# Kernel optimization log

Hardware: AMD Instinct MI355X
Metric: run time of the kernel (lower is better)

The kernel has to match this reference:

```python
import jax, jax.numpy as jnp
import numpy as np

B, D, U = 4096, 256, 512


def setup_inputs() -> dict:
    key = jax.random.key(0)
    k = jax.random.split(key, 7)
    return {
        "x": jax.random.normal(k[0], (B, D), jnp.float32),
        "t": jax.random.uniform(k[1], (B, 1), jnp.float32),           # elapsed-time input
        "h0": jax.random.normal(k[2], (B, U), jnp.float32),
        "c0": jax.random.normal(k[3], (B, U), jnp.float32),
        "kernel": jax.random.normal(k[4], (D, 5 * U), jnp.float32) / np.sqrt(D).astype(np.float32),
        "recurrent_kernel": jax.random.normal(k[5], (U, 3 * U), jnp.float32) / np.sqrt(U).astype(np.float32),
        "kernel_time": jax.random.normal(k[6], (1, 3 * U), jnp.float32) * 0.1,
    }


def reference(x, t, h0, c0, kernel, recurrent_kernel, kernel_time):
    sig = jax.nn.sigmoid
    # Fused input projection: one GEMM instead of 5 (same math, kernel cols are
    # ordered [i, c, o, t1, t2] exactly as the original slices self.kernel).
    x_i, x_c, x_o, x_t1, x_t2 = jnp.split(x @ kernel, 5, axis=1)          # each (B, U)
    # Fused recurrent projection: cols ordered [i, c, o].
    r_i, r_c, r_o = jnp.split(h0 @ recurrent_kernel, 3, axis=1)           # each (B, U)
    # Time projections: cols ordered [t1, t2, o].
    kt1, kt2, kto = jnp.split(t @ kernel_time, 3, axis=1)                 # each (B, U)

    i = sig(x_i + r_i)
    t_1 = sig(x_t1 + sig(kt1))
    # tf.where(t_1 > -1e-5, -1e-5, t_1): sigmoid output is always > -1e-5,
    # so this clamps to the constant -1e-5; keep the where for faithfulness.
    NEG_EPS = jnp.float32(-1e-5)
    t_1_constraint = jnp.where(t_1 > NEG_EPS, jnp.full_like(t_1, NEG_EPS), t_1)
    t_2 = sig(x_t2 + sig(kt2))
    c_tilde = jnp.tanh(x_c + r_c)
    c_m_ = (1.0 - i * t_1) * c0 + i * c_tilde * t_1_constraint
    c_m = (1.0 - i) * c0 + i * c_tilde * t_2
    o = sig(x_o + r_o + kto)
    h = jnp.tanh(c_m_) * o
    # original returns (h, [h, c_m]); h appears twice, so return (h, c_m)
    return (h, c_m)
```

## Files before the change

### kernel.cpp

```cpp
#include <hip/hip_runtime.h>


typedef __attribute__((ext_vector_type(8))) short short8_t;
typedef __attribute__((ext_vector_type(4))) float f32x4_t;
typedef unsigned int u32;

#define B_N 4096
#define D_K 256
#define U_N 512

__device__ __forceinline__ unsigned short f2bf(float f) {
    unsigned int x = __float_as_uint(f);
    unsigned int r = x + 0x7fffu + ((x >> 16) & 1u);
    return (unsigned short)(r >> 16);
}

__device__ __forceinline__ float sigf(float z) {
    return 1.0f / (1.0f + __expf(-z));
}

__device__ __forceinline__ float tanhfast(float z) {
    return 1.0f - 2.0f / (1.0f + __expf(2.0f * z));
}

__device__ __forceinline__ void gl16(const unsigned short* g, unsigned short* l) {
    __builtin_amdgcn_global_load_lds(
        (const __attribute__((address_space(1))) u32*)g,
        (__attribute__((address_space(3))) u32*)l, 16, 0, 0);
}

#define SWZ(r, kc) ((((r) * 8) + ((kc) ^ ((r) & 7))) * 8)

#define WAIT_VM(N)                                            \
    asm volatile("s_waitcnt vmcnt(" #N ")" ::: "memory");     \
    __builtin_amdgcn_sched_barrier(0)

__global__ __launch_bounds__(256) void prep(
    const float* __restrict__ x, const float* __restrict__ h0,
    const float* __restrict__ kern, const float* __restrict__ rk,
    unsigned short* __restrict__ xs, unsigned short* __restrict__ hs,
    unsigned short* __restrict__ ksw, unsigned short* __restrict__ rsw)
{
    const int c = blockIdx.x * 256 + threadIdx.x;
    if (c < 131072) {
        const int t = c >> 10, q = c & 1023;
        const int row = q >> 3, kc = q & 7;
        const int rb = t >> 2, kb = t & 3;
        const float* s = x + (size_t)(rb * 128 + row) * D_K + kb * 64 + kc * 8;
        short8_t o;
#pragma unroll
        for (int j = 0; j < 8; ++j) o[j] = (short)f2bf(s[j]);
        *reinterpret_cast<short8_t*>(xs + (size_t)t * 8192 + SWZ(row, kc)) = o;
    } else if (c < 393216) {
        const int c2 = c - 131072;
        const int t = c2 >> 10, q = c2 & 1023;
        const int row = q >> 3, kc = q & 7;
        const int rb = t >> 3, kb = t & 7;
        const float* s = h0 + (size_t)(rb * 128 + row) * U_N + kb * 64 + kc * 8;
        short8_t o;
#pragma unroll
        for (int j = 0; j < 8; ++j) o[j] = (short)f2bf(s[j]);
        *reinterpret_cast<short8_t*>(hs + (size_t)t * 8192 + SWZ(row, kc)) = o;
    } else if (c < 475136) {
        const int c2 = c - 393216;
        const int t = c2 / 1280, q = c2 - t * 1280;
        const int kc = q / 160, r = q - kc * 160;
        const int nb = t >> 2, kb = t & 3;
        const int col = (r >> 5) * U_N + nb * 32 + (r & 31);
        short8_t o;
#pragma unroll
        for (int j = 0; j < 8; ++j)
            o[j] = (short)f2bf(kern[(size_t)(kb * 64 + kc * 8 + j) * 2560 + col]);
        *reinterpret_cast<short8_t*>(ksw + (size_t)t * 10240 + SWZ(r, kc)) = o;
    } else {
        const int c2 = c - 475136;
        const int t = c2 / 768, q = c2 - t * 768;
        const int kc = q / 96, r = q - kc * 96;
        const int nb = t >> 3, kb = t & 7;
        const int col = (r >> 5) * U_N + nb * 32 + (r & 31);
        short8_t o;
#pragma unroll
        for (int j = 0; j < 8; ++j)
            o[j] = (short)f2bf(rk[(size_t)(kb * 64 + kc * 8 + j) * 1536 + col]);
        *reinterpret_cast<short8_t*>(rsw + (size_t)t * 6144 + SWZ(r, kc)) = o;
    }
}

__global__ __launch_bounds__(512, 2) void tlstm_main(
    const unsigned short* __restrict__ xs,
    const unsigned short* __restrict__ hs,
    const unsigned short* __restrict__ ksw,
    const unsigned short* __restrict__ rsw,
    const float* __restrict__ tvec,
    const float* __restrict__ c0,
    const float* __restrict__ ktime,
    float* __restrict__ out)
{
    __shared__ __align__(16) unsigned short lds[2][28672];

    const int tid = threadIdx.x;
    const int wave = tid >> 6;
    const int lane = tid & 63;
    const int lr = lane & 15;
    const int lq = lane >> 4;
    const int wm = wave >> 2;
    const int wn = wave & 3;
    const int nb = blockIdx.x;
    const int rb = blockIdx.y;

    const int u = nb * 64 + wn * 16 + lr;

    f32x4_t acc[8][4];
#pragma unroll
    for (int m = 0; m < 8; ++m)
#pragma unroll
        for (int p = 0; p < 4; ++p)
            acc[m][p] = (f32x4_t){0.f, 0.f, 0.f, 0.f};

    float c0r[16];

    auto stage = [&](int s, int buf) {
        unsigned short* ab = &lds[buf][0];
        unsigned short* bb = &lds[buf][8192];
        if (s < 4) {
            const unsigned short* at = xs + (size_t)(rb * 4 + s) * 8192;
            gl16(at + (size_t)tid * 8,         ab + (size_t)(wave * 64) * 8);
            gl16(at + (size_t)(512 + tid) * 8, ab + (size_t)(512 + wave * 64) * 8);
            const unsigned short* b0 = ksw + (size_t)(nb * 8 + s) * 10240;
            const unsigned short* b1 = ksw + (size_t)(nb * 8 + 4 + s) * 10240;
#pragma unroll
            for (int j = 0; j < 5; ++j) {
                const int c = j * 512 + tid;
                const unsigned short* src = (c < 1280) ? (b0 + (size_t)c * 8)
                                                       : (b1 + (size_t)(c - 1280) * 8);
                gl16(src, bb + (size_t)(j * 512 + wave * 64) * 8);
            }
        } else {
            const unsigned short* at = hs + (size_t)(rb * 8 + (s - 4)) * 8192;
            gl16(at + (size_t)tid * 8,         ab + (size_t)(wave * 64) * 8);
            gl16(at + (size_t)(512 + tid) * 8, ab + (size_t)(512 + wave * 64) * 8);
            const unsigned short* b0 = rsw + (size_t)(nb * 16 + (s - 4)) * 6144;
            const unsigned short* b1 = rsw + (size_t)(nb * 16 + 8 + (s - 4)) * 6144;
#pragma unroll
            for (int j = 0; j < 3; ++j) {
                const int c = j * 512 + tid;
                const unsigned short* src = (c < 768) ? (b0 + (size_t)c * 8)
                                                      : (b1 + (size_t)(c - 768) * 8);
                gl16(src, bb + (size_t)(j * 512 + wave * 64) * 8);
            }
        }
    };

    auto compute1 = [&](int buf) {
        const unsigned short* ab = &lds[buf][0];
        const unsigned short* bb = &lds[buf][8192];
#pragma unroll
        for (int ks = 0; ks < 2; ++ks) {
            const int kc = ks * 4 + lq;
            short8_t a[4];
#pragma unroll
            for (int p = 0; p < 4; ++p)
                a[p] = *reinterpret_cast<const short8_t*>(ab + SWZ(wm * 64 + p * 16 + lr, kc));
#pragma unroll
            for (int m = 0; m < 5; ++m) {
                const int r = (wn >> 1) * 160 + m * 32 + (wn & 1) * 16 + lr;
                short8_t b = *reinterpret_cast<const short8_t*>(bb + SWZ(r, kc));
#pragma unroll
                for (int p = 0; p < 4; ++p)
                    acc[m][p] = __builtin_amdgcn_mfma_f32_16x16x32_bf16(a[p], b, acc[m][p], 0, 0, 0);
            }
        }
    };

    auto compute2 = [&](int buf) {
        const unsigned short* ab = &lds[buf][0];
        const unsigned short* bb = &lds[buf][8192];
#pragma unroll
        for (int ks = 0; ks < 2; ++ks) {
            const int kc = ks * 4 + lq;
            short8_t a[4];
#pragma unroll
            for (int p = 0; p < 4; ++p)
                a[p] = *reinterpret_cast<const short8_t*>(ab + SWZ(wm * 64 + p * 16 + lr, kc));
#pragma unroll
            for (int m = 0; m < 3; ++m) {
                const int r = (wn >> 1) * 96 + m * 32 + (wn & 1) * 16 + lr;
                short8_t b = *reinterpret_cast<const short8_t*>(bb + SWZ(r, kc));
#pragma unroll
                for (int p = 0; p < 4; ++p)
                    acc[5 + m][p] = __builtin_amdgcn_mfma_f32_16x16x32_bf16(a[p], b, acc[5 + m][p], 0, 0, 0);
            }
        }
    };

#define K_BODY(S, NV, CF)                                  \
    {                                                      \
        WAIT_VM(NV);                                       \
        __builtin_amdgcn_s_barrier();                      \
        __builtin_amdgcn_sched_barrier(0);                 \
        CF((S) & 1);                                       \
        __builtin_amdgcn_sched_barrier(0);                 \
        __builtin_amdgcn_s_barrier();                      \
        __builtin_amdgcn_sched_barrier(0);                 \
    }

    stage(0, 0);
    stage(1, 1);  K_BODY(0, 7,  compute1);
    stage(2, 0);  K_BODY(1, 7,  compute1);
    stage(3, 1);  K_BODY(2, 7,  compute1);
    stage(4, 0);  K_BODY(3, 5,  compute1);
    stage(5, 1);  K_BODY(4, 5,  compute2);
    stage(6, 0);  K_BODY(5, 5,  compute2);
    stage(7, 1);  K_BODY(6, 5,  compute2);
    stage(8, 0);  K_BODY(7, 5,  compute2);
    stage(9, 1);
    asm volatile("" ::: "memory");
#pragma unroll
    for (int p = 0; p < 4; ++p)
#pragma unroll
        for (int i2 = 0; i2 < 4; ++i2) {
            const int b = rb * 128 + wm * 64 + p * 16 + lq * 4 + i2;
            c0r[p * 4 + i2] = c0[(size_t)b * U_N + u];
        }
    K_BODY(8, 21, compute2);
    stage(10, 0); K_BODY(9, 21, compute2);
    stage(11, 1); K_BODY(10, 5, compute2);
    K_BODY(11, 0, compute2);

    const float NEG_EPS = -1e-5f;
    const float kt1 = ktime[u];
    const float kt2 = ktime[U_N + u];
    const float kto = ktime[2 * U_N + u];
#pragma unroll
    for (int p = 0; p < 4; ++p)
#pragma unroll
        for (int i2 = 0; i2 < 4; ++i2) {
            const int b = rb * 128 + wm * 64 + p * 16 + lq * 4 + i2;
            const float tb = tvec[b];
            const float c0v = c0r[p * 4 + i2];
            const float x_i  = acc[0][p][i2];
            const float x_c  = acc[1][p][i2];
            const float x_o  = acc[2][p][i2];
            const float x_t1 = acc[3][p][i2];
            const float x_t2 = acc[4][p][i2];
            const float r_i  = acc[5][p][i2];
            const float r_c  = acc[6][p][i2];
            const float r_o  = acc[7][p][i2];

            const float ig  = sigf(x_i + r_i);
            const float t1v = sigf(x_t1 + sigf(tb * kt1));
            const float t1c = (t1v > NEG_EPS) ? NEG_EPS : t1v;
            const float t2v = sigf(x_t2 + sigf(tb * kt2));
            const float ct  = tanhfast(x_c + r_c);
            const float cm_ = (1.f - ig * t1v) * c0v + ig * ct * t1c;
            const float cm  = (1.f - ig) * c0v + ig * ct * t2v;
            const float og  = sigf(x_o + r_o + tb * kto);

            out[(size_t)b * U_N + u] = tanhfast(cm_) * og;
            out[(size_t)B_N * U_N + (size_t)b * U_N + u] = cm;
        }
}

extern "C" void kernel_launch(void* const* d_in, const int* in_sizes, int n_in,
                              void* d_out, int out_size, void* d_ws, size_t ws_size,
                              hipStream_t stream) {
    const float* x     = (const float*)d_in[0];
    const float* t     = (const float*)d_in[1];
    const float* h0    = (const float*)d_in[2];
    const float* c0    = (const float*)d_in[3];
    const float* kern  = (const float*)d_in[4];
    const float* rk    = (const float*)d_in[5];
    const float* ktime = (const float*)d_in[6];
    float* out = (float*)d_out;

    unsigned short* xs  = (unsigned short*)d_ws;
    unsigned short* hs  = (unsigned short*)((char*)d_ws + 2097152);
    unsigned short* ksw = (unsigned short*)((char*)d_ws + 6291456);
    unsigned short* rsw = (unsigned short*)((char*)d_ws + 7602176);

    prep<<<2240, 256, 0, stream>>>(x, h0, kern, rk, xs, hs, ksw, rsw);
    tlstm_main<<<dim3(8, 32), 512, 0, stream>>>(
        xs, hs, ksw, rsw, t, c0, ktime, out);
}
```

Baseline: 35.80 us.

## Split MFMA k-steps into ping-pong phases with barriers and setprio

Each staged tile's compute is split into two k-phases. Each phase loads all of its LDS fragments up front, then a workgroup barrier and an lgkmcnt wait precede an MFMA burst raised with s_setprio, a ping-pong schedule meant to interleave LDS reads and MFMAs across waves. The c0 prefetch into registers mid-pipeline is dropped in favour of loading c0 directly in the epilogue, which simplifies the vmcnt waits but exposes c0 load latency at the end. The constant-folded t1 clamp removes a compare, and the extra barriers add synchronisation cost.

```diff
diff --git a/kernel.cpp b/kernel.cpp
--- a/kernel.cpp
+++ b/kernel.cpp
@@ -33,6 +33,14 @@
 
 #define WAIT_VM(N)                                            \
     asm volatile("s_waitcnt vmcnt(" #N ")" ::: "memory");     \
+    __builtin_amdgcn_sched_barrier(0)
+
+#define LGKM0                                                 \
+    asm volatile("s_waitcnt lgkmcnt(0)" ::: "memory");        \
+    __builtin_amdgcn_sched_barrier(0)
+
+#define SBAR                                                  \
+    __builtin_amdgcn_s_barrier();                             \
     __builtin_amdgcn_sched_barrier(0)
 
 __global__ __launch_bounds__(256) void prep(
@@ -117,8 +125,6 @@
         for (int p = 0; p < 4; ++p)
             acc[m][p] = (f32x4_t){0.f, 0.f, 0.f, 0.f};
 
-    float c0r[16];
-
     auto stage = [&](int s, int buf) {
         unsigned short* ab = &lds[buf][0];
         unsigned short* bb = &lds[buf][8192];
@@ -151,81 +157,80 @@
         }
     };
 
-    auto compute1 = [&](int buf) {
+    auto phase1 = [&](int buf, int ks) {
         const unsigned short* ab = &lds[buf][0];
         const unsigned short* bb = &lds[buf][8192];
-#pragma unroll
-        for (int ks = 0; ks < 2; ++ks) {
-            const int kc = ks * 4 + lq;
-            short8_t a[4];
+        const int kc = ks * 4 + lq;
+        short8_t a[4], b[5];
+#pragma unroll
+        for (int p = 0; p < 4; ++p)
+            a[p] = *reinterpret_cast<const short8_t*>(ab + SWZ(wm * 64 + p * 16 + lr, kc));
+#pragma unroll
+        for (int m = 0; m < 5; ++m) {
+            const int r = (wn >> 1) * 160 + m * 32 + (wn & 1) * 16 + lr;
+            b[m] = *reinterpret_cast<const short8_t*>(bb + SWZ(r, kc));
+        }
+        __builtin_amdgcn_sched_barrier(0);
+        SBAR;
+        LGKM0;
+        __builtin_amdgcn_s_setprio(1);
+#pragma unroll
+        for (int m = 0; m < 5; ++m)
 #pragma unroll
             for (int p = 0; p < 4; ++p)
-                a[p] = *reinterpret_cast<const short8_t*>(ab + SWZ(wm * 64 + p * 16 + lr, kc));
-#pragma unroll
-            for (int m = 0; m < 5; ++m) {
-                const int r = (wn >> 1) * 160 + m * 32 + (wn & 1) * 16 + lr;
-                short8_t b = *reinterpret_cast<const short8_t*>(bb + SWZ(r, kc));
-#pragma unroll
-                for (int p = 0; p < 4; ++p)
-                    acc[m][p] = __builtin_amdgcn_mfma_f32_16x16x32_bf16(a[p], b, acc[m][p], 0, 0, 0);
-            }
-        }
+                acc[m][p] = __builtin_amdgcn_mfma_f32_16x16x32_bf16(a[p], b[m], acc[m][p], 0, 0, 0);
+        __builtin_amdgcn_s_setprio(0);
+        __builtin_amdgcn_sched_barrier(0);
     };
 
-    auto compute2 = [&](int buf) {
+    auto phase2 = [&](int buf, int ks) {
         const unsigned short* ab = &lds[buf][0];
         const unsigned short* bb = &lds[buf][8192];
-#pragma unroll
-        for (int ks = 0; ks < 2; ++ks) {
-            const int kc = ks * 4 + lq;
-            short8_t a[4];
+        const int kc = ks * 4 + lq;
+        short8_t a[4], b[3];
+#pragma unroll
+        for (int p = 0; p < 4; ++p)
+            a[p] = *reinterpret_cast<const short8_t*>(ab + SWZ(wm * 64 + p * 16 + lr, kc));
+#pragma unroll
+        for (int m = 0; m < 3; ++m) {
+            const int r = (wn >> 1) * 96 + m * 32 + (wn & 1) * 16 + lr;
+            b[m] = *reinterpret_cast<const short8_t*>(bb + SWZ(r, kc));
+        }
+        __builtin_amdgcn_sched_barrier(0);
+        SBAR;
+        LGKM0;
+        __builtin_amdgcn_s_setprio(1);
+#pragma unroll
+        for (int m = 0; m < 3; ++m)
 #pragma unroll
             for (int p = 0; p < 4; ++p)
-                a[p] = *reinterpret_cast<const short8_t*>(ab + SWZ(wm * 64 + p * 16 + lr, kc));
-#pragma unroll
-            for (int m = 0; m < 3; ++m) {
-                const int r = (wn >> 1) * 96 + m * 32 + (wn & 1) * 16 + lr;
-                short8_t b = *reinterpret_cast<const short8_t*>(bb + SWZ(r, kc));
-#pragma unroll
-                for (int p = 0; p < 4; ++p)
-                    acc[5 + m][p] = __builtin_amdgcn_mfma_f32_16x16x32_bf16(a[p], b, acc[5 + m][p], 0, 0, 0);
-            }
-        }
+                acc[5 + m][p] = __builtin_amdgcn_mfma_f32_16x16x32_bf16(a[p], b[m], acc[5 + m][p], 0, 0, 0);
+        __builtin_amdgcn_s_setprio(0);
+        __builtin_amdgcn_sched_barrier(0);
     };
 
-#define K_BODY(S, NV, CF)                                  \
+#define K_BODY(S, NV, PH)                                  \
     {                                                      \
         WAIT_VM(NV);                                       \
-        __builtin_amdgcn_s_barrier();                      \
-        __builtin_amdgcn_sched_barrier(0);                 \
-        CF((S) & 1);                                       \
-        __builtin_amdgcn_sched_barrier(0);                 \
-        __builtin_amdgcn_s_barrier();                      \
-        __builtin_amdgcn_sched_barrier(0);                 \
+        SBAR;                                              \
+        PH((S) & 1, 0);                                    \
+        PH((S) & 1, 1);                                    \
+        SBAR;                                              \
     }
 
     stage(0, 0);
-    stage(1, 1);  K_BODY(0, 7,  compute1);
-    stage(2, 0);  K_BODY(1, 7,  compute1);
-    stage(3, 1);  K_BODY(2, 7,  compute1);
-    stage(4, 0);  K_BODY(3, 5,  compute1);
-    stage(5, 1);  K_BODY(4, 5,  compute2);
-    stage(6, 0);  K_BODY(5, 5,  compute2);
-    stage(7, 1);  K_BODY(6, 5,  compute2);
-    stage(8, 0);  K_BODY(7, 5,  compute2);
-    stage(9, 1);
-    asm volatile("" ::: "memory");
-#pragma unroll
-    for (int p = 0; p < 4; ++p)
-#pragma unroll
-        for (int i2 = 0; i2 < 4; ++i2) {
-            const int b = rb * 128 + wm * 64 + p * 16 + lq * 4 + i2;
-            c0r[p * 4 + i2] = c0[(size_t)b * U_N + u];
-        }
-    K_BODY(8, 21, compute2);
-    stage(10, 0); K_BODY(9, 21, compute2);
-    stage(11, 1); K_BODY(10, 5, compute2);
-    K_BODY(11, 0, compute2);
+    stage(1, 1);   K_BODY(0, 7, phase1);
+    stage(2, 0);   K_BODY(1, 7, phase1);
+    stage(3, 1);   K_BODY(2, 7, phase1);
+    stage(4, 0);   K_BODY(3, 5, phase1);
+    stage(5, 1);   K_BODY(4, 5, phase2);
+    stage(6, 0);   K_BODY(5, 5, phase2);
+    stage(7, 1);   K_BODY(6, 5, phase2);
+    stage(8, 0);   K_BODY(7, 5, phase2);
+    stage(9, 1);   K_BODY(8, 5, phase2);
+    stage(10, 0);  K_BODY(9, 5, phase2);
+    stage(11, 1);  K_BODY(10, 5, phase2);
+    K_BODY(11, 0, phase2);
 
     const float NEG_EPS = -1e-5f;
     const float kt1 = ktime[u];
@@ -237,7 +242,7 @@
         for (int i2 = 0; i2 < 4; ++i2) {
             const int b = rb * 128 + wm * 64 + p * 16 + lq * 4 + i2;
             const float tb = tvec[b];
-            const float c0v = c0r[p * 4 + i2];
+            const float c0v = c0[(size_t)b * U_N + u];
             const float x_i  = acc[0][p][i2];
             const float x_c  = acc[1][p][i2];
             const float x_o  = acc[2][p][i2];
@@ -249,10 +254,9 @@
 
             const float ig  = sigf(x_i + r_i);
             const float t1v = sigf(x_t1 + sigf(tb * kt1));
-            const float t1c = (t1v > NEG_EPS) ? NEG_EPS : t1v;
             const float t2v = sigf(x_t2 + sigf(tb * kt2));
             const float ct  = tanhfast(x_c + r_c);
-            const float cm_ = (1.f - ig * t1v) * c0v + ig * ct * t1c;
+            const float cm_ = (1.f - ig * t1v) * c0v + ig * ct * NEG_EPS;
             const float cm  = (1.f - ig) * c0v + ig * ct * t2v;
             const float og  = sigf(x_o + r_o + tb * kto);
 
```

Result: faster. 34.67 us (-3.1%).
